# Kernel tuning notes

Measured on AMD Instinct MI355X. Metric: run time of the kernel, lower is better.

## Reference

```python
import jax, jax.numpy as jnp
import numpy as np

NUM_HEADS = 12
SCALE = 0.125  # (C // num_heads) ** -0.5 = 64 ** -0.5


def setup_inputs() -> dict:
    key = jax.random.key(0)
    k1, k2, k3, k4, k5 = jax.random.split(key, 5)
    B, N, C = 8, 1024, 768
    x = jax.random.normal(k1, (B, N, C), dtype=jnp.float32)
    qkv_w = jax.random.normal(k2, (3 * C, C), dtype=jnp.float32) * (C ** -0.5)
    qkv_b = jax.random.normal(k3, (3 * C,), dtype=jnp.float32) * 0.02
    proj_w = jax.random.normal(k4, (C, C), dtype=jnp.float32) * (C ** -0.5)
    proj_b = jax.random.normal(k5, (C,), dtype=jnp.float32) * 0.02
    return {"x": x, "qkv_w": qkv_w, "qkv_b": qkv_b,
            "proj_w": proj_w, "proj_b": proj_b, "H": 32, "W": 32}


def reference(x, qkv_w, qkv_b, proj_w, proj_b, H, W):
    B, N, C = x.shape
    hd = C // NUM_HEADS
    # qkv: [B, N, 3C] -> [3, B, heads, N, hd]
    qkv = (x @ qkv_w.T + qkv_b).reshape(B, N, 3, NUM_HEADS, hd)
    qkv = jnp.transpose(qkv, (2, 0, 3, 1, 4))
    q, k, v = qkv[0], qkv[1], qkv[2]
    # attention scores [B, heads, N, N]
    attn = jnp.einsum('bhnd,bhmd->bhnm', q, k) * SCALE
    attn = jax.nn.softmax(attn, axis=-1)
    # attn_drop / proj_drop are identity in eval mode
    out = jnp.einsum('bhnm,bhmd->bhnd', attn, v)
    out = jnp.transpose(out, (0, 2, 1, 3)).reshape(B, N, C)
    out = out @ proj_w.T + proj_b
    return out
```

## Files before the change

kernel.cpp:

```cpp
#include <hip/hip_runtime.h>
#include <math.h>

#define NSEQ  1024
#define CDIM  768
#define NH    12
#define HD    64
#define QS    6291456
#define EXPC  0.18033688011112042f

typedef __bf16 bf16x8 __attribute__((ext_vector_type(8)));
typedef float  f32x4  __attribute__((ext_vector_type(4)));

__device__ __forceinline__ unsigned short f2bf(float f) {
    union { float f; unsigned u; } v; v.f = f;
    unsigned r = v.u + 0x7FFFu + ((v.u >> 16) & 1u);
    return (unsigned short)(r >> 16);
}

__device__ __forceinline__ unsigned pk_hi16(unsigned a, unsigned b) {
    return __builtin_amdgcn_perm(b, a, 0x07060302u);
}
__device__ __forceinline__ uint2 pack4bf_trunc(float p0, float p1, float p2, float p3) {
    return make_uint2(pk_hi16(__float_as_uint(p0), __float_as_uint(p1)),
                      pk_hi16(__float_as_uint(p2), __float_as_uint(p3)));
}

__device__ __forceinline__ void gld_lds16(const unsigned short* g, unsigned short* l) {
    __builtin_amdgcn_global_load_lds(
        (const __attribute__((address_space(1))) void*)g,
        (__attribute__((address_space(3))) void*)l, 16, 0, 0);
}

__global__ __launch_bounds__(256) void cvt_all(const float* __restrict__ x,
                                               const float* __restrict__ w1,
                                               const float* __restrict__ w2,
                                               unsigned short* __restrict__ xb,
                                               unsigned short* __restrict__ w1b,
                                               unsigned short* __restrict__ w2b,
                                               int n0, int n1, int n2) {
    int i = (blockIdx.x * 256 + threadIdx.x) * 4;
    const float* s; unsigned short* d; int off;
    if (i < n0)           { s = x;  d = xb;  off = i; }
    else if (i < n0 + n1) { s = w1; d = w1b; off = i - n0; }
    else if (i < n0 + n1 + n2) { s = w2; d = w2b; off = i - n0 - n1; }
    else return;
    float4 v = *(const float4*)(s + off);
    ushort4 o;
    o.x = f2bf(v.x); o.y = f2bf(v.y); o.z = f2bf(v.z); o.w = f2bf(v.w);
    *(ushort4*)(d + off) = o;
}

template <int MODE>
__global__ __launch_bounds__(256) void mfma_gemm_bt(const unsigned short* __restrict__ A,
                                                    const unsigned short* __restrict__ Bw,
                                                    const float* __restrict__ bias,
                                                    void* __restrict__ outp,
                                                    int M, int N, int K) {
    __shared__ unsigned short smem[4 * 128 * 32];

    const int tid = threadIdx.x;
    const int wave = tid >> 6, lane = tid & 63;
    const int row16 = lane & 15, quad = lane >> 4;
    const int wm = (wave >> 1) * 64, wn = (wave & 1) * 64;
    const int m0 = blockIdx.x * 128, n0 = blockIdx.y * 128;

    const int srow0 = (tid * 8) >> 5,         scol0 = (tid * 8) & 31;
    const int srow1 = ((tid + 256) * 8) >> 5, scol1 = ((tid + 256) * 8) & 31;

    f32x4 acc[4][4];
#pragma unroll
    for (int i = 0; i < 4; ++i)
#pragma unroll
        for (int j = 0; j < 4; ++j) acc[i][j] = (f32x4){0.f, 0.f, 0.f, 0.f};

    gld_lds16(&A[(size_t)(m0 + srow0) * K + scol0], &smem[wave * 512]);
    gld_lds16(&A[(size_t)(m0 + srow1) * K + scol1], &smem[2048 + wave * 512]);
    gld_lds16(&Bw[(size_t)(n0 + srow0) * K + scol0], &smem[8192 + wave * 512]);
    gld_lds16(&Bw[(size_t)(n0 + srow1) * K + scol1], &smem[8192 + 2048 + wave * 512]);

    const int nk = K / 32;
    for (int ki = 0; ki < nk; ++ki) {
        const int co = (ki & 1) * 4096;
        const int no = 4096 - co;
        __syncthreads();
        if (ki + 1 < nk) {
            const int k0 = (ki + 1) * 32;
            gld_lds16(&A[(size_t)(m0 + srow0) * K + k0 + scol0], &smem[no + wave * 512]);
            gld_lds16(&A[(size_t)(m0 + srow1) * K + k0 + scol1], &smem[no + 2048 + wave * 512]);
            gld_lds16(&Bw[(size_t)(n0 + srow0) * K + k0 + scol0], &smem[8192 + no + wave * 512]);
            gld_lds16(&Bw[(size_t)(n0 + srow1) * K + k0 + scol1], &smem[8192 + no + 2048 + wave * 512]);
        }
        bf16x8 af[4], bfr[4];
#pragma unroll
        for (int mt = 0; mt < 4; ++mt)
            af[mt] = *(const bf16x8*)&smem[co + (wm + mt * 16 + row16) * 32 + quad * 8];
#pragma unroll
        for (int nt = 0; nt < 4; ++nt)
            bfr[nt] = *(const bf16x8*)&smem[8192 + co + (wn + nt * 16 + row16) * 32 + quad * 8];
#pragma unroll
        for (int mt = 0; mt < 4; ++mt)
#pragma unroll
            for (int nt = 0; nt < 4; ++nt)
                acc[mt][nt] = __builtin_amdgcn_mfma_f32_16x16x32_bf16(af[mt], bfr[nt], acc[mt][nt], 0, 0, 0);
    }

    if (MODE == 0) {
        float bias4[4];
#pragma unroll
        for (int nt = 0; nt < 4; ++nt) bias4[nt] = bias[n0 + wn + nt * 16 + row16];
#pragma unroll
        for (int mt = 0; mt < 4; ++mt)
#pragma unroll
            for (int nt = 0; nt < 4; ++nt)
#pragma unroll
                for (int r = 0; r < 4; ++r) {
                    int grow = m0 + wm + mt * 16 + quad * 4 + r;
                    int gcol = n0 + wn + nt * 16 + row16;
                    ((float*)outp)[(size_t)grow * N + gcol] = acc[mt][nt][r] + bias4[nt];
                }
    } else {
        float scv[4], bsv[4];
#pragma unroll
        for (int nt = 0; nt < 4; ++nt) {
            int gc = n0 + wn + nt * 16 + row16;
            float sc = (gc < CDIM) ? EXPC : 1.0f;
            scv[nt] = sc;
            bsv[nt] = bias[gc] * sc;
        }
        unsigned short* qkvb = (unsigned short*)outp;
        __syncthreads();
#pragma unroll
        for (int mt = 0; mt < 4; ++mt)
#pragma unroll
            for (int nt = 0; nt < 4; ++nt)
#pragma unroll
                for (int r = 0; r < 4; ++r)
                    smem[(wm + mt * 16 + quad * 4 + r) * 128 + wn + nt * 16 + row16] =
                        f2bf(fmaf(acc[mt][nt][r], scv[nt], bsv[nt]));
        __syncthreads();
#pragma unroll
        for (int i = 0; i < 8; ++i) {
            int u4 = i * 256 + tid;
            int row = u4 >> 4;
            int c8 = u4 & 15;
            int grow = m0 + row;
            int gcol = n0 + c8 * 8;
            int t = gcol / CDIM;
            int rr = gcol - t * CDIM;
            int h = rr >> 6, d = rr & 63;
            int b = grow >> 10, n = grow & 1023;
            *(uint4*)&qkvb[(size_t)t * QS + ((((size_t)b * NH + h) << 10) + n) * 64 + d] =
                *(const uint4*)&smem[row * 128 + c8 * 8];
        }
    }
}

__global__ __launch_bounds__(256, 4) void attn_mfma(const unsigned short* __restrict__ qkv,
                                                    unsigned short* __restrict__ abuf) {
    __shared__ unsigned short Ks[64 * 72];
    __shared__ unsigned short Vt[64 * 72];
    __shared__ unsigned short Ps[4][32 * 72];

    const int tid = threadIdx.x;
    const int wave = tid >> 6, lane = tid & 63;
    const int row16 = lane & 15, quad = lane >> 4;
    const int bid = blockIdx.x;
    const int xcd = bid & 7;
    const int local = bid >> 3;
    const int bh = xcd * 12 + (local >> 3);
    const int qt = local & 7;

    const unsigned short* Qg = qkv + (size_t)bh * NSEQ * HD + (size_t)qt * 128 * HD;
    const unsigned short* Kg = qkv + (size_t)QS + (size_t)bh * NSEQ * HD;
    const unsigned short* Vg = qkv + (size_t)2 * QS + (size_t)bh * NSEQ * HD;

    bf16x8 aq[2][2];
#pragma unroll
    for (int mt = 0; mt < 2; ++mt)
#pragma unroll
        for (int kst = 0; kst < 2; ++kst)
            aq[mt][kst] = *(const bf16x8*)&Qg[(size_t)(wave * 32 + mt * 16 + row16) * 64 +
                                              kst * 32 + quad * 8];

    f32x4 o[2][4];
    float l_i[2] = {0.f, 0.f};
#pragma unroll
    for (int mt = 0; mt < 2; ++mt)
#pragma unroll
        for (int j = 0; j < 4; ++j) o[mt][j] = (f32x4){0.f, 0.f, 0.f, 0.f};

    const int krow0 = (tid * 8) >> 6,  kcol0 = (tid * 8) & 63;
    const int krow1 = ((tid + 256) * 8) >> 6, kcol1 = ((tid + 256) * 8) & 63;
    const int kpair = tid & 31;
    const int colc = tid >> 5;

    uint4 ka = *(const uint4*)&Kg[(size_t)krow0 * 64 + kcol0];
    uint4 kb = *(const uint4*)&Kg[(size_t)krow1 * 64 + kcol1];
    uint4 va = *(const uint4*)&Vg[(size_t)(2 * kpair) * 64 + colc * 8];
    uint4 vb = *(const uint4*)&Vg[(size_t)(2 * kpair + 1) * 64 + colc * 8];

    for (int kt = 0; kt < 16; ++kt) {
        __syncthreads();
        *(uint4*)&Ks[krow0 * 72 + kcol0] = ka;
        *(uint4*)&Ks[krow1 * 72 + kcol1] = kb;
        {
            const unsigned* pa = (const unsigned*)&va;
            const unsigned* pb = (const unsigned*)&vb;
            unsigned int* vt32 = (unsigned int*)Vt;
#pragma unroll
            for (int jj = 0; jj < 4; ++jj) {
                vt32[(colc * 8 + 2 * jj)     * 36 + kpair] =
                    __builtin_amdgcn_perm(pb[jj], pa[jj], 0x05040100u);
                vt32[(colc * 8 + 2 * jj + 1) * 36 + kpair] =
                    __builtin_amdgcn_perm(pb[jj], pa[jj], 0x07060302u);
            }
        }
        __syncthreads();

        if (kt < 15) {
            const unsigned short* kn = Kg + (size_t)(kt + 1) * 64 * 64;
            const unsigned short* vn = Vg + (size_t)(kt + 1) * 64 * 64;
            ka = *(const uint4*)&kn[(size_t)krow0 * 64 + kcol0];
            kb = *(const uint4*)&kn[(size_t)krow1 * 64 + kcol1];
            va = *(const uint4*)&vn[(size_t)(2 * kpair) * 64 + colc * 8];
            vb = *(const uint4*)&vn[(size_t)(2 * kpair + 1) * 64 + colc * 8];
        }

        f32x4 st[4][2];
#pragma unroll
        for (int nt = 0; nt < 4; ++nt)
#pragma unroll
            for (int mt = 0; mt < 2; ++mt) st[nt][mt] = (f32x4){0.f, 0.f, 0.f, 0.f};
#pragma unroll
        for (int kst = 0; kst < 2; ++kst) {
            bf16x8 ak[4];
#pragma unroll
            for (int nt = 0; nt < 4; ++nt)
                ak[nt] = *(const bf16x8*)&Ks[(nt * 16 + row16) * 72 + kst * 32 + quad * 8];
#pragma unroll
            for (int nt = 0; nt < 4; ++nt)
#pragma unroll
                for (int mt = 0; mt < 2; ++mt)
                    st[nt][mt] = __builtin_amdgcn_mfma_f32_16x16x32_bf16(ak[nt], aq[mt][kst], st[nt][mt], 0, 0, 0);
        }

#pragma unroll
        for (int mt = 0; mt < 2; ++mt)
#pragma unroll
            for (int nt = 0; nt < 4; ++nt) {
                float p0 = __builtin_amdgcn_exp2f(st[nt][mt][0]);
                float p1 = __builtin_amdgcn_exp2f(st[nt][mt][1]);
                float p2 = __builtin_amdgcn_exp2f(st[nt][mt][2]);
                float p3 = __builtin_amdgcn_exp2f(st[nt][mt][3]);
                l_i[mt] += (p0 + p1) + (p2 + p3);
                *(uint2*)&Ps[wave][(mt * 16 + row16) * 72 + nt * 16 + quad * 4] =
                    pack4bf_trunc(p0, p1, p2, p3);
            }

#pragma unroll
        for (int kst = 0; kst < 2; ++kst) {
            bf16x8 ap[2], bv[4];
#pragma unroll
            for (int mt = 0; mt < 2; ++mt)
                ap[mt] = *(const bf16x8*)&Ps[wave][(mt * 16 + row16) * 72 + kst * 32 + quad * 8];
#pragma unroll
            for (int dt = 0; dt < 4; ++dt)
                bv[dt] = *(const bf16x8*)&Vt[(dt * 16 + row16) * 72 + kst * 32 + quad * 8];
#pragma unroll
            for (int mt = 0; mt < 2; ++mt)
#pragma unroll
                for (int dt = 0; dt < 4; ++dt)
                    o[mt][dt] = __builtin_amdgcn_mfma_f32_16x16x32_bf16(ap[mt], bv[dt], o[mt][dt], 0, 0, 0);
        }
    }

    const int b = bh / NH, h = bh - b * NH;
#pragma unroll
    for (int mt = 0; mt < 2; ++mt) {
        float l = l_i[mt];
        l += __shfl_xor(l, 16);
        l += __shfl_xor(l, 32);
#pragma unroll
        for (int r = 0; r < 4; ++r) {
            float inv = 1.f / __shfl(l, quad * 4 + r);
            int n = qt * 128 + wave * 32 + mt * 16 + quad * 4 + r;
            size_t base = ((size_t)(b * NSEQ + n)) * CDIM + h * HD;
#pragma unroll
            for (int dt = 0; dt < 4; ++dt)
                abuf[base + dt * 16 + row16] = f2bf(o[mt][dt][r] * inv);
        }
    }
}

extern "C" void kernel_launch(void* const* d_in, const int* in_sizes, int n_in,
                              void* d_out, int out_size, void* d_ws, size_t ws_size,
                              hipStream_t stream) {
    const float* x      = (const float*)d_in[0];
    const float* qkv_w  = (const float*)d_in[1];
    const float* qkv_b  = (const float*)d_in[2];
    const float* proj_w = (const float*)d_in[3];
    const float* proj_b = (const float*)d_in[4];
    float* out = (float*)d_out;

    const int M = 8 * NSEQ;
    unsigned short* ws = (unsigned short*)d_ws;
    unsigned short* xb   = ws;
    unsigned short* wq   = xb + (size_t)M * CDIM;
    unsigned short* wp   = wq + (size_t)3 * CDIM * CDIM;
    unsigned short* qkvb = wp + (size_t)CDIM * CDIM;
    unsigned short* ab   = qkvb + (size_t)3 * QS;

    const int nx = M * CDIM, nq = 3 * CDIM * CDIM, np = CDIM * CDIM;
    cvt_all<<<(nx + nq + np) / 1024, 256, 0, stream>>>(x, qkv_w, proj_w, xb, wq, wp,
                                                       nx, nq, np);

    mfma_gemm_bt<1><<<dim3(M / 128, (3 * CDIM) / 128), 256, 0, stream>>>(
        xb, wq, qkv_b, qkvb, M, 3 * CDIM, CDIM);

    attn_mfma<<<dim3(8 * NH * (NSEQ / 128)), 256, 0, stream>>>(qkvb, ab);

    mfma_gemm_bt<0><<<dim3(M / 128, CDIM / 128), 256, 0, stream>>>(
        ab, wp, proj_b, out, M, CDIM, CDIM);
}
```

Baseline: 183.3 us.

## Double attention query tile per block to 256 rows for more K/V reuse

Each attention block now processes 256 query rows (64 per wave) instead of 128, halving the grid and the number of times each K/V tile is loaded and transposed into shared memory. K fragments are loaded once per tile and reused across four query sub-tiles, with per-subtile score computation to bound register use. Launch bounds drop to 2 blocks per CU since register and LDS usage per block grow. The trade-off is fewer blocks (384) and lower occupancy, with less latency hiding.

```diff
diff --git a/kernel.cpp b/kernel.cpp
--- a/kernel.cpp
+++ b/kernel.cpp
@@ -155,11 +155,11 @@
     }
 }
 
-__global__ __launch_bounds__(256, 4) void attn_mfma(const unsigned short* __restrict__ qkv,
+__global__ __launch_bounds__(256, 2) void attn_mfma(const unsigned short* __restrict__ qkv,
                                                     unsigned short* __restrict__ abuf) {
     __shared__ unsigned short Ks[64 * 72];
     __shared__ unsigned short Vt[64 * 72];
-    __shared__ unsigned short Ps[4][32 * 72];
+    __shared__ unsigned short Ps[4][64 * 72];
 
     const int tid = threadIdx.x;
     const int wave = tid >> 6, lane = tid & 63;
@@ -167,25 +167,25 @@
     const int bid = blockIdx.x;
     const int xcd = bid & 7;
     const int local = bid >> 3;
-    const int bh = xcd * 12 + (local >> 3);
-    const int qt = local & 7;
-
-    const unsigned short* Qg = qkv + (size_t)bh * NSEQ * HD + (size_t)qt * 128 * HD;
+    const int bh = xcd * 12 + (local >> 2);
+    const int qt = local & 3;
+
+    const unsigned short* Qg = qkv + (size_t)bh * NSEQ * HD + (size_t)qt * 256 * HD;
     const unsigned short* Kg = qkv + (size_t)QS + (size_t)bh * NSEQ * HD;
     const unsigned short* Vg = qkv + (size_t)2 * QS + (size_t)bh * NSEQ * HD;
 
-    bf16x8 aq[2][2];
-#pragma unroll
-    for (int mt = 0; mt < 2; ++mt)
+    bf16x8 aq[4][2];
+#pragma unroll
+    for (int mt = 0; mt < 4; ++mt)
 #pragma unroll
         for (int kst = 0; kst < 2; ++kst)
-            aq[mt][kst] = *(const bf16x8*)&Qg[(size_t)(wave * 32 + mt * 16 + row16) * 64 +
+            aq[mt][kst] = *(const bf16x8*)&Qg[(size_t)(wave * 64 + mt * 16 + row16) * 64 +
                                               kst * 32 + quad * 8];
 
-    f32x4 o[2][4];
-    float l_i[2] = {0.f, 0.f};
-#pragma unroll
-    for (int mt = 0; mt < 2; ++mt)
+    f32x4 o[4][4];
+    float l_i[4] = {0.f, 0.f, 0.f, 0.f};
+#pragma unroll
+    for (int mt = 0; mt < 4; ++mt)
 #pragma unroll
         for (int j = 0; j < 4; ++j) o[mt][j] = (f32x4){0.f, 0.f, 0.f, 0.f};
 
@@ -198,6 +198,8 @@
     uint4 kb = *(const uint4*)&Kg[(size_t)krow1 * 64 + kcol1];
     uint4 va = *(const uint4*)&Vg[(size_t)(2 * kpair) * 64 + colc * 8];
     uint4 vb = *(const uint4*)&Vg[(size_t)(2 * kpair + 1) * 64 + colc * 8];
+
+    unsigned short* Psw = &Ps[wave][0];
 
     for (int kt = 0; kt < 16; ++kt) {
         __syncthreads();
@@ -226,48 +228,46 @@
             vb = *(const uint4*)&vn[(size_t)(2 * kpair + 1) * 64 + colc * 8];
         }
 
-        f32x4 st[4][2];
-#pragma unroll
-        for (int nt = 0; nt < 4; ++nt)
-#pragma unroll
-            for (int mt = 0; mt < 2; ++mt) st[nt][mt] = (f32x4){0.f, 0.f, 0.f, 0.f};
-#pragma unroll
-        for (int kst = 0; kst < 2; ++kst) {
-            bf16x8 ak[4];
+        bf16x8 ak[2][4];
+#pragma unroll
+        for (int kst = 0; kst < 2; ++kst)
 #pragma unroll
             for (int nt = 0; nt < 4; ++nt)
-                ak[nt] = *(const bf16x8*)&Ks[(nt * 16 + row16) * 72 + kst * 32 + quad * 8];
-#pragma unroll
-            for (int nt = 0; nt < 4; ++nt)
-#pragma unroll
-                for (int mt = 0; mt < 2; ++mt)
-                    st[nt][mt] = __builtin_amdgcn_mfma_f32_16x16x32_bf16(ak[nt], aq[mt][kst], st[nt][mt], 0, 0, 0);
-        }
-
-#pragma unroll
-        for (int mt = 0; mt < 2; ++mt)
+                ak[kst][nt] = *(const bf16x8*)&Ks[(nt * 16 + row16) * 72 + kst * 32 + quad * 8];
+
+#pragma unroll
+        for (int mt = 0; mt < 4; ++mt) {
+            f32x4 st[4];
+#pragma unroll
+            for (int nt = 0; nt < 4; ++nt) st[nt] = (f32x4){0.f, 0.f, 0.f, 0.f};
+#pragma unroll
+            for (int kst = 0; kst < 2; ++kst)
+#pragma unroll
+                for (int nt = 0; nt < 4; ++nt)
+                    st[nt] = __builtin_amdgcn_mfma_f32_16x16x32_bf16(ak[kst][nt], aq[mt][kst], st[nt], 0, 0, 0);
 #pragma unroll
             for (int nt = 0; nt < 4; ++nt) {
-                float p0 = __builtin_amdgcn_exp2f(st[nt][mt][0]);
-                float p1 = __builtin_amdgcn_exp2f(st[nt][mt][1]);
-                float p2 = __builtin_amdgcn_exp2f(st[nt][mt][2]);
-                float p3 = __builtin_amdgcn_exp2f(st[nt][mt][3]);
+                float p0 = __builtin_amdgcn_exp2f(st[nt][0]);
+                float p1 = __builtin_amdgcn_exp2f(st[nt][1]);
+                float p2 = __builtin_amdgcn_exp2f(st[nt][2]);
+                float p3 = __builtin_amdgcn_exp2f(st[nt][3]);
                 l_i[mt] += (p0 + p1) + (p2 + p3);
-                *(uint2*)&Ps[wave][(mt * 16 + row16) * 72 + nt * 16 + quad * 4] =
+                *(uint2*)&Psw[(mt * 16 + row16) * 72 + nt * 16 + quad * 4] =
                     pack4bf_trunc(p0, p1, p2, p3);
             }
+        }
 
 #pragma unroll
         for (int kst = 0; kst < 2; ++kst) {
-            bf16x8 ap[2], bv[4];
-#pragma unroll
-            for (int mt = 0; mt < 2; ++mt)
-                ap[mt] = *(const bf16x8*)&Ps[wave][(mt * 16 + row16) * 72 + kst * 32 + quad * 8];
+            bf16x8 bv[4], ap[4];
 #pragma unroll
             for (int dt = 0; dt < 4; ++dt)
                 bv[dt] = *(const bf16x8*)&Vt[(dt * 16 + row16) * 72 + kst * 32 + quad * 8];
 #pragma unroll
-            for (int mt = 0; mt < 2; ++mt)
+            for (int mt = 0; mt < 4; ++mt)
+                ap[mt] = *(const bf16x8*)&Psw[(mt * 16 + row16) * 72 + kst * 32 + quad * 8];
+#pragma unroll
+            for (int mt = 0; mt < 4; ++mt)
 #pragma unroll
                 for (int dt = 0; dt < 4; ++dt)
                     o[mt][dt] = __builtin_amdgcn_mfma_f32_16x16x32_bf16(ap[mt], bv[dt], o[mt][dt], 0, 0, 0);
@@ -276,14 +276,14 @@
 
     const int b = bh / NH, h = bh - b * NH;
 #pragma unroll
-    for (int mt = 0; mt < 2; ++mt) {
+    for (int mt = 0; mt < 4; ++mt) {
         float l = l_i[mt];
         l += __shfl_xor(l, 16);
         l += __shfl_xor(l, 32);
 #pragma unroll
         for (int r = 0; r < 4; ++r) {
             float inv = 1.f / __shfl(l, quad * 4 + r);
-            int n = qt * 128 + wave * 32 + mt * 16 + quad * 4 + r;
+            int n = qt * 256 + wave * 64 + mt * 16 + quad * 4 + r;
             size_t base = ((size_t)(b * NSEQ + n)) * CDIM + h * HD;
 #pragma unroll
             for (int dt = 0; dt < 4; ++dt)
@@ -317,7 +317,7 @@
     mfma_gemm_bt<1><<<dim3(M / 128, (3 * CDIM) / 128), 256, 0, stream>>>(
         xb, wq, qkv_b, qkvb, M, 3 * CDIM, CDIM);
 
-    attn_mfma<<<dim3(8 * NH * (NSEQ / 128)), 256, 0, stream>>>(qkvb, ab);
+    attn_mfma<<<dim3(8 * NH * (NSEQ / 256)), 256, 0, stream>>>(qkvb, ab);
 
     mfma_gemm_bt<0><<<dim3(M / 128, CDIM / 128), 256, 0, stream>>>(
         ab, wp, proj_b, out, M, CDIM, CDIM);
```

Result: slower. 187.4 us (+2.3%).
